# Optimization experiments

Measured on AMD Instinct MI355X. Metric: run time of the kernel, lower is better.

## Reference

```python
import jax, jax.numpy as jnp
import numpy as np

N, E, H, S = 50000, 400000, 128, 3  # nodes, edges, hidden_dim, mp steps
NODE_IN, EDGE_IN, OUT = 4, 3, 2


def _mlp(x, W1, b1, W2, b2, W3, b3):
    # MLP(in, [H, H], out): Linear->ReLU->Linear->ReLU->Linear
    h = jax.nn.relu(x @ W1 + b1)
    h = jax.nn.relu(h @ W2 + b2)
    return h @ W3 + b3


def setup_inputs() -> dict:
    key = jax.random.key(0)
    ks = iter(jax.random.split(key, 64))

    def p(shape):
        fan_in = shape[-2]
        return (jax.random.normal(next(ks), shape, jnp.float32) / np.float32(np.sqrt(fan_in)))

    inp = {}
    inp["x"] = jax.random.normal(next(ks), (N, NODE_IN), jnp.float32)
    inp["edge_attr"] = jax.random.normal(next(ks), (E, EDGE_IN), jnp.float32)
    inp["edge_index"] = jax.random.randint(next(ks), (2, E), 0, N, jnp.int32)
    # node encoder MLP(NODE_IN,[H,H],H)
    inp["ne_W1"], inp["ne_b1"] = p((NODE_IN, H)), jnp.zeros((H,), jnp.float32)
    inp["ne_W2"], inp["ne_b2"] = p((H, H)), jnp.zeros((H,), jnp.float32)
    inp["ne_W3"], inp["ne_b3"] = p((H, H)), jnp.zeros((H,), jnp.float32)
    # edge encoder MLP(EDGE_IN,[H,H],H)
    inp["ee_W1"], inp["ee_b1"] = p((EDGE_IN, H)), jnp.zeros((H,), jnp.float32)
    inp["ee_W2"], inp["ee_b2"] = p((H, H)), jnp.zeros((H,), jnp.float32)
    inp["ee_W3"], inp["ee_b3"] = p((H, H)), jnp.zeros((H,), jnp.float32)
    # processor: per-step edge MLP(3H,[H,H],H) and node MLP(2H,[H,H],H), stacked over S
    inp["pe_W1"], inp["pe_b1"] = p((S, 3 * H, H)), jnp.zeros((S, H), jnp.float32)
    inp["pe_W2"], inp["pe_b2"] = p((S, H, H)), jnp.zeros((S, H), jnp.float32)
    inp["pe_W3"], inp["pe_b3"] = p((S, H, H)), jnp.zeros((S, H), jnp.float32)
    inp["pn_W1"], inp["pn_b1"] = p((S, 2 * H, H)), jnp.zeros((S, H), jnp.float32)
    inp["pn_W2"], inp["pn_b2"] = p((S, H, H)), jnp.zeros((S, H), jnp.float32)
    inp["pn_W3"], inp["pn_b3"] = p((S, H, H)), jnp.zeros((S, H), jnp.float32)
    # node decoder MLP(H,[H,H],OUT)
    inp["nd_W1"], inp["nd_b1"] = p((H, H)), jnp.zeros((H,), jnp.float32)
    inp["nd_W2"], inp["nd_b2"] = p((H, H)), jnp.zeros((H,), jnp.float32)
    inp["nd_W3"], inp["nd_b3"] = p((H, OUT)), jnp.zeros((OUT,), jnp.float32)
    return inp


def reference(x, edge_attr, edge_index,
              ne_W1, ne_b1, ne_W2, ne_b2, ne_W3, ne_b3,
              ee_W1, ee_b1, ee_W2, ee_b2, ee_W3, ee_b3,
              pe_W1, pe_b1, pe_W2, pe_b2, pe_W3, pe_b3,
              pn_W1, pn_b1, pn_W2, pn_b2, pn_W3, pn_b3,
              nd_W1, nd_b1, nd_W2, nd_b2, nd_W3, nd_b3):
    src, dst = edge_index[0], edge_index[1]
    # encode
    h = _mlp(x, ne_W1, ne_b1, ne_W2, ne_b2, ne_W3, ne_b3)          # [N, H]
    e = _mlp(edge_attr, ee_W1, ee_b1, ee_W2, ee_b2, ee_W3, ee_b3)  # [E, H]
    # processor: gather -> edge MLP (residual) -> scatter-sum -> node MLP (residual)
    for t in range(S):
        m_in = jnp.concatenate([h[src], h[dst], e], axis=-1)        # [E, 3H]
        e = e + _mlp(m_in, pe_W1[t], pe_b1[t], pe_W2[t], pe_b2[t], pe_W3[t], pe_b3[t])
        agg = jax.ops.segment_sum(e, dst, num_segments=N)           # [N, H]
        n_in = jnp.concatenate([h, agg], axis=-1)                   # [N, 2H]
        h = h + _mlp(n_in, pn_W1[t], pn_b1[t], pn_W2[t], pn_b2[t], pn_W3[t], pn_b3[t])
    # decode
    return _mlp(h, nd_W1, nd_b1, nd_W2, nd_b2, nd_W3, nd_b3)        # [N, OUT]
```

## Files before the change

kernel.cpp:

```cpp
#include <hip/hip_runtime.h>
#include <hip/hip_bf16.h>
#include <cstddef>

#define NND 50000
#define NNDP 50048
#define NED 400000
#define HD 128
#define NSTEP 3
#define NSB 196
#define NWP 32

using u16 = unsigned short;
typedef __attribute__((ext_vector_type(8))) short bf16x8;
typedef __attribute__((ext_vector_type(4))) float f32x4;

__device__ __forceinline__ u16 f2b(float f) {
    __hip_bfloat16 b = __float2bfloat16(f);
    union { __hip_bfloat16 b; u16 u; } v; v.b = b;
    return v.u;
}
__device__ __forceinline__ float b2f(u16 u) {
    union { unsigned u; float f; } v; v.u = ((unsigned)u) << 16;
    return v.f;
}

template <int RT>
__device__ __forceinline__ void zero_accs(f32x4 (&acc)[RT][4]) {
    #pragma unroll
    for (int g = 0; g < RT; g++)
        #pragma unroll
        for (int i = 0; i < 4; i++) acc[g][i] = (f32x4)(0.0f);
}

__device__ __forceinline__ void mfma4T(bf16x8 act, const bf16x8 (&wf)[4], f32x4 (&accr)[4]) {
    accr[0] = __builtin_amdgcn_mfma_f32_16x16x32_bf16(wf[0], act, accr[0], 0, 0, 0);
    accr[1] = __builtin_amdgcn_mfma_f32_16x16x32_bf16(wf[1], act, accr[1], 0, 0, 0);
    accr[2] = __builtin_amdgcn_mfma_f32_16x16x32_bf16(wf[2], act, accr[2], 0, 0, 0);
    accr[3] = __builtin_amdgcn_mfma_f32_16x16x32_bf16(wf[3], act, accr[3], 0, 0, 0);
}

__device__ __forceinline__ void load_w16(const u16* __restrict__ Wf, int wc, int lane,
                                         bf16x8 (&wB)[16]) {
    const u16* bp = Wf + (size_t)(wc * 16) * 512 + lane * 8;
    #pragma unroll
    for (int i = 0; i < 16; i++) wB[i] = *(const bf16x8*)(bp + i * 512);
}

template <int RT>
__device__ __forceinline__ void gemm_reg_T(const u16* t, int rbase, const bf16x8 (&wB)[16],
                                           int lane, f32x4 (&acc)[RT][4]) {
    const int cl = lane & 15, q8 = (lane >> 4) * 8;
    #pragma unroll
    for (int k0 = 0; k0 < 4; k0++) {
        const bf16x8 wf[4] = {wB[k0], wB[4 + k0], wB[8 + k0], wB[12 + k0]};
        #pragma unroll
        for (int rt = 0; rt < RT; rt++) {
            bf16x8 a = *(const bf16x8*)(t + (rbase + rt * 16 + cl) * 136 + k0 * 32 + q8);
            mfma4T(a, wf, acc[rt]);
        }
    }
}

template <int KC, int RT>
__device__ __forceinline__ void gemm_lds_T(const u16* t, int rbase,
                                           const u16* __restrict__ Wf,
                                           int wc, int lane, f32x4 (&acc)[RT][4]) {
    const int cl = lane & 15, q8 = (lane >> 4) * 8;
    const u16* bp = Wf + (size_t)(wc * 4 * KC) * 512 + lane * 8;
    #pragma unroll
    for (int k0 = 0; k0 < KC; k0++) {
        bf16x8 wf[4];
        #pragma unroll
        for (int ct = 0; ct < 4; ct++) wf[ct] = *(const bf16x8*)(bp + (ct * KC + k0) * 512);
        #pragma unroll
        for (int rt = 0; rt < RT; rt++) {
            bf16x8 a = *(const bf16x8*)(t + (rbase + rt * 16 + cl) * 136 + k0 * 32 + q8);
            mfma4T(a, wf, acc[rt]);
        }
    }
}

template <int RT, bool RELU>
__device__ __forceinline__ void store_T(u16* T, int rbase, int wc, int lane,
        const f32x4 (&acc)[RT][4], const float* __restrict__ bias) {
    const int cl = lane & 15, q = lane >> 4;
    float4 bv[4];
    #pragma unroll
    for (int ct = 0; ct < 4; ct++)
        bv[ct] = *(const float4*)(bias + wc * 64 + ct * 16 + q * 4);
    #pragma unroll
    for (int rt = 0; rt < RT; rt++) {
        const int row = rbase + rt * 16 + cl;
        #pragma unroll
        for (int ct = 0; ct < 4; ct++) {
            float v0 = acc[rt][ct][0] + bv[ct].x;
            float v1 = acc[rt][ct][1] + bv[ct].y;
            float v2 = acc[rt][ct][2] + bv[ct].z;
            float v3 = acc[rt][ct][3] + bv[ct].w;
            if (RELU) {
                v0 = fmaxf(v0, 0.f); v1 = fmaxf(v1, 0.f);
                v2 = fmaxf(v2, 0.f); v3 = fmaxf(v3, 0.f);
            }
            uint2 pk;
            pk.x = (unsigned)f2b(v0) | ((unsigned)f2b(v1) << 16);
            pk.y = (unsigned)f2b(v2) | ((unsigned)f2b(v3) << 16);
            *(uint2*)(T + row * 136 + wc * 64 + ct * 16 + q * 4) = pk;
        }
    }
}

template <int RT>
__device__ __forceinline__ void store_T_perm(u16* T, int rbase, int wc, int lane,
        const f32x4 (&acc)[RT][4]) {
    const int cl = lane & 15, q = lane >> 4;
    #pragma unroll
    for (int rt = 0; rt < RT; rt++) {
        const int row = rbase + rt * 16 + cl;
        #pragma unroll
        for (int ct = 0; ct < 4; ct++) {
            uint2 pk;
            pk.x = (unsigned)f2b(acc[rt][ct][0]) | ((unsigned)f2b(acc[rt][ct][1]) << 16);
            pk.y = (unsigned)f2b(acc[rt][ct][2]) | ((unsigned)f2b(acc[rt][ct][3]) << 16);
            *(uint2*)(T + row * 136 + wc * 64 + q * 16 + ct * 4) = pk;
        }
    }
}

template <int RT>
__device__ __forceinline__ void epi_plain(const u16* T, u16* __restrict__ base, int row0,
        int rbase, int nrows, int wc, int lane) {
    #pragma unroll
    for (int p = 0; p < RT * 2; p++) {
        const int lrow = rbase + p * 8 + (lane >> 3);
        const int col = wc * 64 + (lane & 7) * 8;
        const int grow = row0 + lrow;
        if (grow < nrows) {
            bf16x8 tv = *(const bf16x8*)(T + lrow * 136 + col);
            *(bf16x8*)(base + (size_t)grow * HD + col) = tv;
        }
    }
}

__global__ void count_kernel(const int* __restrict__ eidx, int* __restrict__ counts) {
    int i = blockIdx.x * 256 + threadIdx.x;
    if (i < NED) atomicAdd(&counts[eidx[NED + i]], 1);
}

__global__ __launch_bounds__(256) void bsum_kernel(const int* __restrict__ counts,
                                                   int* __restrict__ bsum) {
    __shared__ int sm[256];
    const int i = threadIdx.x, b = blockIdx.x;
    const int idx = b * 256 + i;
    sm[i] = (idx < NNDP) ? counts[idx] : 0;
    __syncthreads();
    for (int ofs = 128; ofs > 0; ofs >>= 1) {
        if (i < ofs) sm[i] += sm[i + ofs];
        __syncthreads();
    }
    if (i == 0) bsum[b] = sm[0];
}

__global__ __launch_bounds__(256) void bscan_kernel(const int* __restrict__ bsum,
                                                    int* __restrict__ bbase,
                                                    int* __restrict__ offsets) {
    __shared__ int sm[256];
    const int i = threadIdx.x;
    int v = (i < NSB) ? bsum[i] : 0;
    sm[i] = v;
    __syncthreads();
    for (int ofs = 1; ofs < 256; ofs <<= 1) {
        int t = (i >= ofs) ? sm[i - ofs] : 0;
        __syncthreads();
        sm[i] += t;
        __syncthreads();
    }
    if (i < NSB) bbase[i] = sm[i] - v;
    if (i == NSB - 1) offsets[NNDP] = sm[i];
}

__global__ __launch_bounds__(256) void blocal_kernel(const int* __restrict__ counts,
                                                     const int* __restrict__ bbase,
                                                     int* __restrict__ offsets,
                                                     int* __restrict__ cursors) {
    __shared__ int sm[256];
    const int i = threadIdx.x, b = blockIdx.x;
    const int idx = b * 256 + i;
    int v = (idx < NNDP) ? counts[idx] : 0;
    sm[i] = v;
    __syncthreads();
    for (int ofs = 1; ofs < 256; ofs <<= 1) {
        int t = (i >= ofs) ? sm[i - ofs] : 0;
        __syncthreads();
        sm[i] += t;
        __syncthreads();
    }
    if (idx < NNDP) {
        int excl = sm[i] - v + bbase[b];
        offsets[idx] = excl;
        cursors[idx] = excl;
    }
}

__global__ void fill_kernel(const int* __restrict__ eidx, int* __restrict__ cursors,
                            int4* __restrict__ epk) {
    int i = blockIdx.x * 256 + threadIdx.x;
    if (i >= NED) return;
    int d = eidx[NED + i];
    int pos = atomicAdd(&cursors[d], 1);
    int4 v; v.x = eidx[i]; v.y = d; v.z = i; v.w = 0;
    epk[pos] = v;
}

struct WPall {
    const float* s[NWP];
    u16* d[NWP];
    int K[NWP];
    int Kp[NWP];
};

__global__ void wprep_all(WPall a) {
    const int wi = blockIdx.y;
    const int Kp = a.Kp[wi];
    int idx = blockIdx.x * 256 + threadIdx.x;
    if (idx >= 128 * Kp) return;
    const int K = a.K[wi];
    const float* __restrict__ src = a.s[wi];
    int j = idx & 7, lane = (idx >> 3) & 63, rest = idx >> 9;
    int KC = Kp >> 5;
    int k0 = rest % KC, n0 = rest / KC;
    int n = n0 * 16 + (lane & 15);
    int k = k0 * 32 + (lane >> 4) * 8 + j;
    float v = (k < K) ? src[(size_t)k * 128 + n] : 0.0f;
    a.d[wi][idx] = f2b(v);
}

__global__ __launch_bounds__(256, 2) void pnode_mfma(
    const u16* __restrict__ h,
    const u16* __restrict__ WsF, const u16* __restrict__ WdF,
    u16* __restrict__ Ps, u16* __restrict__ Pd) {
    __shared__ u16 t1[64 * 136];
    const int tid = threadIdx.x;
    const int lane = tid & 63, w = tid >> 6, wr = w >> 1, wc = w & 1;
    const int cl = lane & 15, q8 = (lane >> 4) * 8;
    const int row0 = blockIdx.x * 64;
    const int rbase = wr * 32;

    bf16x8 aA[2][4];
    #pragma unroll
    for (int rt = 0; rt < 2; rt++) {
        const u16* hp = h + (size_t)(row0 + rbase + rt * 16 + cl) * HD + q8;
        #pragma unroll
        for (int k0 = 0; k0 < 4; k0++) aA[rt][k0] = *(const bf16x8*)(hp + k0 * 32);
    }
    bf16x8 wB[16];
    f32x4 acc[2][4];

    load_w16(WsF, wc, lane, wB);
    zero_accs<2>(acc);
    #pragma unroll
    for (int k0 = 0; k0 < 4; k0++) {
        const bf16x8 wf[4] = {wB[k0], wB[4 + k0], wB[8 + k0], wB[12 + k0]};
        #pragma unroll
        for (int rt = 0; rt < 2; rt++) mfma4T(aA[rt][k0], wf, acc[rt]);
    }
    store_T_perm<2>(t1, rbase, wc, lane, acc);
    epi_plain<2>(t1, Ps, row0, rbase, NNDP, wc, lane);

    load_w16(WdF, wc, lane, wB);
    zero_accs<2>(acc);
    #pragma unroll
    for (int k0 = 0; k0 < 4; k0++) {
        const bf16x8 wf[4] = {wB[k0], wB[4 + k0], wB[8 + k0], wB[12 + k0]};
        #pragma unroll
        for (int rt = 0; rt < 2; rt++) mfma4T(aA[rt][k0], wf, acc[rt]);
    }
    store_T_perm<2>(t1, rbase, wc, lane, acc);
    epi_plain<2>(t1, Pd, row0, rbase, NNDP, wc, lane);
}

__global__ __launch_bounds__(256, 4) void enc_mfma(
    const float* __restrict__ in, int Kin, int nrows, const int4* __restrict__ epk,
    const u16* __restrict__ W1f, const float* __restrict__ b1,
    const u16* __restrict__ W2f, const float* __restrict__ b2,
    const u16* __restrict__ W3f, const float* __restrict__ b3,
    u16* __restrict__ out) {
    __shared__ u16 t1[64 * 136];
    __shared__ u16 t2[64 * 136];
    const int tid = threadIdx.x;
    const int lane = tid & 63, w = tid >> 6, wr = w >> 1, wc = w & 1;
    const int cl = lane & 15, q8 = (lane >> 4) * 8;
    const int row0 = blockIdx.x * 64;
    const int rbase = wr * 32;

    f32x4 acc[2][4];
    zero_accs<2>(acc);
    bf16x8 a[2];
    #pragma unroll
    for (int rt = 0; rt < 2; rt++) {
        a[rt] = (bf16x8){0, 0, 0, 0, 0, 0, 0, 0};
        int grow = row0 + rbase + rt * 16 + cl;
        if (q8 == 0 && grow < nrows) {
            int irow = epk ? epk[grow].z : grow;
            const float* xr = in + (size_t)irow * Kin;
            if (Kin == 4) {
                float4 v = *(const float4*)xr;
                a[rt][0] = (short)f2b(v.x); a[rt][1] = (short)f2b(v.y);
                a[rt][2] = (short)f2b(v.z); a[rt][3] = (short)f2b(v.w);
            } else {
                a[rt][0] = (short)f2b(xr[0]); a[rt][1] = (short)f2b(xr[1]);
                a[rt][2] = (short)f2b(xr[2]);
            }
        }
    }
    {
        const u16* b1p = W1f + (size_t)(wc * 4) * 512 + lane * 8;
        bf16x8 wf[4];
        #pragma unroll
        for (int ct = 0; ct < 4; ct++) wf[ct] = *(const bf16x8*)(b1p + ct * 512);
        #pragma unroll
        for (int rt = 0; rt < 2; rt++) mfma4T(a[rt], wf, acc[rt]);
    }
    store_T<2, true>(t1, rbase, wc, lane, acc, b1);
    __syncthreads();
    zero_accs<2>(acc);
    gemm_lds_T<4, 2>(t1, rbase, W2f, wc, lane, acc);
    store_T<2, true>(t2, rbase, wc, lane, acc, b2);
    __syncthreads();
    zero_accs<2>(acc);
    gemm_lds_T<4, 2>(t2, rbase, W3f, wc, lane, acc);
    store_T<2, false>(t1, rbase, wc, lane, acc, b3);
    epi_plain<2>(t1, out, row0, rbase, nrows, wc, lane);
}

__global__ __launch_bounds__(256, 2) void edge_mfma(
    u16* __restrict__ e, const int4* __restrict__ epk,
    const u16* __restrict__ Ps, const u16* __restrict__ Pd,
    const u16* __restrict__ W1eF, const float* __restrict__ b1,
    const u16* __restrict__ W2f, const float* __restrict__ b2,
    const u16* __restrict__ W3f, const float* __restrict__ b3) {
    __shared__ u16 t1[128 * 136];
    __shared__ u16 t2[128 * 136];
    const int tid = threadIdx.x;
    const int lane = tid & 63, w = tid >> 6, wr = w >> 1, wc = w & 1;
    const int cl = lane & 15, q = lane >> 4, q8 = q * 8;
    const int row0 = blockIdx.x * 128;
    const int rbase = wr * 64;

    bf16x8 wB[16];
    load_w16(W2f, wc, lane, wB);

    int srcv[4], dstv[4];
    const u16* epv[4];
    #pragma unroll
    for (int rt = 0; rt < 4; rt++) {
        int myrow = row0 + rbase + rt * 16 + cl;
        int4 pk = epk[myrow];
        srcv[rt] = pk.x; dstv[rt] = pk.y;
        epv[rt] = e + (size_t)myrow * HD + q8;
    }

    const int pofs = wc * 64 + q * 16;
    f32x4 acc[4][4];
    #pragma unroll
    for (int rt = 0; rt < 4; rt++) {
        const u16* ps = Ps + (size_t)srcv[rt] * HD + pofs;
        const u16* pd = Pd + (size_t)dstv[rt] * HD + pofs;
        bf16x8 a0 = *(const bf16x8*)ps;
        bf16x8 a1 = *(const bf16x8*)(ps + 8);
        bf16x8 b0 = *(const bf16x8*)pd;
        bf16x8 b1v = *(const bf16x8*)(pd + 8);
        #pragma unroll
        for (int ct = 0; ct < 2; ct++)
            #pragma unroll
            for (int i = 0; i < 4; i++)
                acc[rt][ct][i] = b2f((u16)a0[ct * 4 + i]) + b2f((u16)b0[ct * 4 + i]);
        #pragma unroll
        for (int ct = 2; ct < 4; ct++)
            #pragma unroll
            for (int i = 0; i < 4; i++)
                acc[rt][ct][i] = b2f((u16)a1[(ct - 2) * 4 + i]) + b2f((u16)b1v[(ct - 2) * 4 + i]);
    }
    const u16* b1p = W1eF + (size_t)(wc * 16) * 512 + lane * 8;
    #pragma unroll
    for (int k0 = 0; k0 < 4; k0++) {
        bf16x8 wf[4];
        #pragma unroll
        for (int ct = 0; ct < 4; ct++) wf[ct] = *(const bf16x8*)(b1p + (ct * 4 + k0) * 512);
        #pragma unroll
        for (int rt = 0; rt < 4; rt++) {
            bf16x8 a = *(const bf16x8*)(epv[rt] + k0 * 32);
            mfma4T(a, wf, acc[rt]);
        }
    }
    store_T<4, true>(t1, rbase, wc, lane, acc, b1);
    __syncthreads();
    zero_accs<4>(acc);
    gemm_reg_T<4>(t1, rbase, wB, lane, acc);
    load_w16(W3f, wc, lane, wB);
    store_T<4, true>(t2, rbase, wc, lane, acc, b2);
    __syncthreads();
    bf16x8 eold[8];
    #pragma unroll
    for (int p = 0; p < 8; p++) {
        const int lrow = rbase + p * 8 + (lane >> 3);
        const int col = wc * 64 + (lane & 7) * 8;
        eold[p] = *(const bf16x8*)(e + (size_t)(row0 + lrow) * HD + col);
    }
    zero_accs<4>(acc);
    gemm_reg_T<4>(t2, rbase, wB, lane, acc);
    store_T<4, false>(t1, rbase, wc, lane, acc, b3);
    #pragma unroll
    for (int p = 0; p < 8; p++) {
        const int lrow = rbase + p * 8 + (lane >> 3);
        const int col = wc * 64 + (lane & 7) * 8;
        bf16x8 tv = *(const bf16x8*)(t1 + lrow * 136 + col);
        bf16x8 res;
        #pragma unroll
        for (int k = 0; k < 8; k++)
            res[k] = (short)f2b(b2f((u16)tv[k]) + b2f((u16)eold[p][k]));
        *(bf16x8*)(e + (size_t)(row0 + lrow) * HD + col) = res;
    }
}

__global__ __launch_bounds__(256, 3) void node_mfma(
    u16* __restrict__ h, const u16* __restrict__ e, const int* __restrict__ offsets,
    const u16* __restrict__ W1f, const float* __restrict__ b1,
    const u16* __restrict__ W2f, const float* __restrict__ b2,
    const u16* __restrict__ W3f, const float* __restrict__ b3,
    const u16* __restrict__ W1sNx, const u16* __restrict__ W1dNx,
    u16* __restrict__ Ps, u16* __restrict__ Pd) {
    __shared__ u16 tb[64 * 136];
    __shared__ u16 aggT[64 * 136];
    const int tid = threadIdx.x;
    const int lane = tid & 63, w = tid >> 6, wr = w >> 1, wc = w & 1;
    const int cl = lane & 15, q8 = (lane >> 4) * 8;
    const int row0 = blockIdx.x * 64;
    const int rbase = wr * 32;

    {
        const int r = tid >> 2, sgi = tid & 3;
        const int node = row0 + r;
        const int beg = offsets[node], end = offsets[node + 1];
        float s[32];
        #pragma unroll
        for (int k = 0; k < 32; k++) s[k] = 0.0f;
        const u16* ebase = e + sgi * 32;
        int j = beg;
        for (; j + 2 <= end; j += 2) {
            const bf16x8* e0 = (const bf16x8*)(ebase + (size_t)j * HD);
            const bf16x8* e1 = (const bf16x8*)(ebase + (size_t)(j + 1) * HD);
            bf16x8 v0 = e0[0], v1 = e0[1], v2 = e0[2], v3 = e0[3];
            bf16x8 u0 = e1[0], u1 = e1[1], u2 = e1[2], u3 = e1[3];
            #pragma unroll
            for (int k = 0; k < 8; k++) {
                s[k]      += b2f((u16)v0[k]) + b2f((u16)u0[k]);
                s[8 + k]  += b2f((u16)v1[k]) + b2f((u16)u1[k]);
                s[16 + k] += b2f((u16)v2[k]) + b2f((u16)u2[k]);
                s[24 + k] += b2f((u16)v3[k]) + b2f((u16)u3[k]);
            }
        }
        if (j < end) {
            const bf16x8* e0 = (const bf16x8*)(ebase + (size_t)j * HD);
            bf16x8 v0 = e0[0], v1 = e0[1], v2 = e0[2], v3 = e0[3];
            #pragma unroll
            for (int k = 0; k < 8; k++) {
                s[k]      += b2f((u16)v0[k]);
                s[8 + k]  += b2f((u16)v1[k]);
                s[16 + k] += b2f((u16)v2[k]);
                s[24 + k] += b2f((u16)v3[k]);
            }
        }
        #pragma unroll
        for (int q = 0; q < 4; q++) {
            bf16x8 o;
            #pragma unroll
            for (int k = 0; k < 8; k++) o[k] = (short)f2b(s[q * 8 + k]);
            *(bf16x8*)(aggT + r * 136 + sgi * 32 + q * 8) = o;
        }
    }
    __syncthreads();

    f32x4 acc[2][4];
    zero_accs<2>(acc);
    const u16* b1p = W1f + (size_t)(wc * 32) * 512 + lane * 8;
    const u16* hp[2];
    #pragma unroll
    for (int rt = 0; rt < 2; rt++)
        hp[rt] = h + (size_t)(row0 + rbase + rt * 16 + cl) * HD + q8;
    #pragma unroll
    for (int k0 = 0; k0 < 4; k0++) {
        bf16x8 wf[4];
        #pragma unroll
        for (int ct = 0; ct < 4; ct++) wf[ct] = *(const bf16x8*)(b1p + (ct * 8 + k0) * 512);
        #pragma unroll
        for (int rt = 0; rt < 2; rt++) {
            bf16x8 a = *(const bf16x8*)(hp[rt] + k0 * 32);
            mfma4T(a, wf, acc[rt]);
        }
    }
    #pragma unroll
    for (int k0 = 0; k0 < 4; k0++) {
        bf16x8 wf[4];
        #pragma unroll
        for (int ct = 0; ct < 4; ct++) wf[ct] = *(const bf16x8*)(b1p + (ct * 8 + 4 + k0) * 512);
        #pragma unroll
        for (int rt = 0; rt < 2; rt++) {
            bf16x8 a = *(const bf16x8*)(aggT + (rbase + rt * 16 + cl) * 136 + k0 * 32 + q8);
            mfma4T(a, wf, acc[rt]);
        }
    }
    store_T<2, true>(tb, rbase, wc, lane, acc, b1);
    __syncthreads();
    zero_accs<2>(acc);
    gemm_lds_T<4, 2>(tb, rbase, W2f, wc, lane, acc);
    store_T<2, true>(aggT, rbase, wc, lane, acc, b2);
    __syncthreads();
    bf16x8 hold[4];
    #pragma unroll
    for (int p = 0; p < 4; p++) {
        const int lrow = rbase + p * 8 + (lane >> 3);
        const int col = wc * 64 + (lane & 7) * 8;
        hold[p] = *(const bf16x8*)(h + (size_t)(row0 + lrow) * HD + col);
    }
    zero_accs<2>(acc);
    gemm_lds_T<4, 2>(aggT, rbase, W3f, wc, lane, acc);
    store_T<2, false>(tb, rbase, wc, lane, acc, b3);
    #pragma unroll
    for (int p = 0; p < 4; p++) {
        const int lrow = rbase + p * 8 + (lane >> 3);
        const int col = wc * 64 + (lane & 7) * 8;
        bf16x8 tv = *(const bf16x8*)(tb + lrow * 136 + col);
        bf16x8 res;
        #pragma unroll
        for (int k = 0; k < 8; k++)
            res[k] = (short)f2b(b2f((u16)tv[k]) + b2f((u16)hold[p][k]));
        *(bf16x8*)(h + (size_t)(row0 + lrow) * HD + col) = res;
        *(bf16x8*)(tb + lrow * 136 + col) = res;
    }
    if (W1sNx) {
        __syncthreads();
        bf16x8 wB[16];
        load_w16(W1sNx, wc, lane, wB);
        f32x4 pac[2][4];
        zero_accs<2>(pac);
        gemm_reg_T<2>(tb, rbase, wB, lane, pac);
        store_T_perm<2>(aggT, rbase, wc, lane, pac);
        epi_plain<2>(aggT, Ps, row0, rbase, NNDP, wc, lane);
        load_w16(W1dNx, wc, lane, wB);
        zero_accs<2>(pac);
        gemm_reg_T<2>(tb, rbase, wB, lane, pac);
        store_T_perm<2>(aggT, rbase, wc, lane, pac);
        epi_plain<2>(aggT, Pd, row0, rbase, NNDP, wc, lane);
    }
}

__global__ __launch_bounds__(256, 4) void dec_mfma(
    const u16* __restrict__ h,
    const u16* __restrict__ W1f, const float* __restrict__ b1,
    const u16* __restrict__ W2f, const float* __restrict__ b2,
    const float* __restrict__ W3, const float* __restrict__ b3,
    float* __restrict__ out) {
    __shared__ u16 t1[32 * 136];
    __shared__ u16 t2[32 * 136];
    const int tid = threadIdx.x;
    const int lane = tid & 63, w = tid >> 6, wr = w >> 1, wc = w & 1;
    const int cl = lane & 15, q8 = (lane >> 4) * 8;
    const int row0 = blockIdx.x * 32;
    const int rbase = wr * 16;
    const u16* hp = h + (size_t)(row0 + rbase + cl) * HD + q8;

    f32x4 acc[1][4];
    zero_accs<1>(acc);
    const u16* b1p = W1f + (size_t)(wc * 16) * 512 + lane * 8;
    #pragma unroll
    for (int k0 = 0; k0 < 4; k0++) {
        bf16x8 wf[4];
        #pragma unroll
        for (int ct = 0; ct < 4; ct++) wf[ct] = *(const bf16x8*)(b1p + (ct * 4 + k0) * 512);
        bf16x8 a = *(const bf16x8*)(hp + k0 * 32);
        mfma4T(a, wf, acc[0]);
    }
    store_T<1, true>(t1, rbase, wc, lane, acc, b1);
    __syncthreads();
    zero_accs<1>(acc);
    gemm_lds_T<4, 1>(t1, rbase, W2f, wc, lane, acc);
    store_T<1, true>(t2, rbase, wc, lane, acc, b2);
    __syncthreads();
    if (tid < 64) {
        const int rr = tid >> 1, o = tid & 1;
        const int grow = row0 + rr;
        if (grow < NND) {
            float a = b3[o];
            for (int k = 0; k < HD; k++) a += b2f(t2[rr * 136 + k]) * W3[k * 2 + o];
            out[(size_t)grow * 2 + o] = a;
        }
    }
}

extern "C" void kernel_launch(void* const* d_in, const int* in_sizes, int n_in,
                              void* d_out, int out_size, void* d_ws, size_t ws_size,
                              hipStream_t stream) {
    (void)in_sizes; (void)n_in; (void)out_size; (void)ws_size;
    const float* x    = (const float*)d_in[0];
    const float* eatt = (const float*)d_in[1];
    const int*   eidx = (const int*)d_in[2];
    const float *neW1 = (const float*)d_in[3],  *neb1 = (const float*)d_in[4];
    const float *neW2 = (const float*)d_in[5],  *neb2 = (const float*)d_in[6];
    const float *neW3 = (const float*)d_in[7],  *neb3 = (const float*)d_in[8];
    const float *eeW1 = (const float*)d_in[9],  *eeb1 = (const float*)d_in[10];
    const float *eeW2 = (const float*)d_in[11], *eeb2 = (const float*)d_in[12];
    const float *eeW3 = (const float*)d_in[13], *eeb3 = (const float*)d_in[14];
    const float *peW1 = (const float*)d_in[15], *peb1 = (const float*)d_in[16];
    const float *peW2 = (const float*)d_in[17], *peb2 = (const float*)d_in[18];
    const float *peW3 = (const float*)d_in[19], *peb3 = (const float*)d_in[20];
    const float *pnW1 = (const float*)d_in[21], *pnb1 = (const float*)d_in[22];
    const float *pnW2 = (const float*)d_in[23], *pnb2 = (const float*)d_in[24];
    const float *pnW3 = (const float*)d_in[25], *pnb3 = (const float*)d_in[26];
    const float *ndW1 = (const float*)d_in[27], *ndb1 = (const float*)d_in[28];
    const float *ndW2 = (const float*)d_in[29], *ndb2 = (const float*)d_in[30];
    const float *ndW3 = (const float*)d_in[31], *ndb3 = (const float*)d_in[32];

    char* ws = (char*)d_ws;
    u16*   h       = (u16*)ws;
    u16*   e       = (u16*)(ws + 12812288);
    int*   bsum    = (int*)(ws + 115212288);
    int*   bbase   = (int*)(ws + 115213312);
    int*   counts  = (int*)(ws + 115245056);
    int*   cursors = (int*)(ws + 115445248);
    int*   offsets = (int*)(ws + 115645440);
    int4*  epk     = (int4*)(ws + 115845760);
    u16*   Ps      = (u16*)(ws + 122245760);
    u16*   Pd      = (u16*)(ws + 135058048);
    u16*   wts     = (u16*)(ws + 147870336);

    u16* p = wts;
    u16 *neW1t = p; p += 128 * 32;
    u16 *neW2t = p; p += 128 * 128;
    u16 *neW3t = p; p += 128 * 128;
    u16 *eeW1t = p; p += 128 * 32;
    u16 *eeW2t = p; p += 128 * 128;
    u16 *eeW3t = p; p += 128 * 128;
    u16 *peW1sF[NSTEP], *peW1dF[NSTEP], *peW1eF[NSTEP], *peW2t[NSTEP], *peW3t[NSTEP];
    u16 *pnW1t[NSTEP], *pnW2t[NSTEP], *pnW3t[NSTEP];
    for (int t = 0; t < NSTEP; t++) {
        peW1sF[t] = p; p += 128 * 128;
        peW1dF[t] = p; p += 128 * 128;
        peW1eF[t] = p; p += 128 * 128;
        peW2t[t]  = p; p += 128 * 128;
        peW3t[t]  = p; p += 128 * 128;
    }
    for (int t = 0; t < NSTEP; t++) {
        pnW1t[t] = p; p += 128 * 256;
        pnW2t[t] = p; p += 128 * 128;
        pnW3t[t] = p; p += 128 * 128;
    }
    u16 *ndW1t = p; p += 128 * 128;
    u16 *ndW2t = p; p += 128 * 128;

    hipMemsetAsync(counts, 0, NNDP * sizeof(int), stream);
    count_kernel<<<(NED + 255) / 256, 256, 0, stream>>>(eidx, counts);
    bsum_kernel<<<NSB, 256, 0, stream>>>(counts, bsum);
    bscan_kernel<<<1, 256, 0, stream>>>(bsum, bbase, offsets);
    blocal_kernel<<<NSB, 256, 0, stream>>>(counts, bbase, offsets, cursors);
    fill_kernel<<<(NED + 255) / 256, 256, 0, stream>>>(eidx, cursors, epk);

    WPall wa;
    int wn = 0;
    auto ADD = [&](const float* s, u16* d, int K, int Kp) {
        wa.s[wn] = s; wa.d[wn] = d; wa.K[wn] = K; wa.Kp[wn] = Kp; wn++;
    };
    ADD(neW1, neW1t, 4, 32);
    ADD(neW2, neW2t, 128, 128);
    ADD(neW3, neW3t, 128, 128);
    ADD(eeW1, eeW1t, 3, 32);
    ADD(eeW2, eeW2t, 128, 128);
    ADD(eeW3, eeW3t, 128, 128);
    for (int t = 0; t < NSTEP; t++) {
        const float* base = peW1 + (size_t)t * 384 * 128;
        ADD(base,             peW1sF[t], 128, 128);
        ADD(base + 128 * 128, peW1dF[t], 128, 128);
        ADD(base + 256 * 128, peW1eF[t], 128, 128);
        ADD(peW2 + (size_t)t * 128 * 128, peW2t[t], 128, 128);
        ADD(peW3 + (size_t)t * 128 * 128, peW3t[t], 128, 128);
        ADD(pnW1 + (size_t)t * 256 * 128, pnW1t[t], 256, 256);
        ADD(pnW2 + (size_t)t * 128 * 128, pnW2t[t], 128, 128);
        ADD(pnW3 + (size_t)t * 128 * 128, pnW3t[t], 128, 128);
    }
    ADD(ndW1, ndW1t, 128, 128);
    ADD(ndW2, ndW2t, 128, 128);
    wprep_all<<<dim3(128, NWP), 256, 0, stream>>>(wa);

    enc_mfma<<<NNDP / 64, 256, 0, stream>>>(x, 4, NND, nullptr,
                                            neW1t, neb1, neW2t, neb2, neW3t, neb3, h);
    enc_mfma<<<NED / 64, 256, 0, stream>>>(eatt, 3, NED, epk,
                                           eeW1t, eeb1, eeW2t, eeb2, eeW3t, eeb3, e);
    pnode_mfma<<<NNDP / 64, 256, 0, stream>>>(h, peW1sF[0], peW1dF[0], Ps, Pd);

    for (int t = 0; t < NSTEP; t++) {
        edge_mfma<<<NED / 128, 256, 0, stream>>>(
            e, epk, Ps, Pd,
            peW1eF[t], peb1 + (size_t)t * HD,
            peW2t[t],  peb2 + (size_t)t * HD,
            peW3t[t],  peb3 + (size_t)t * HD);
        const bool last = (t + 1 == NSTEP);
        node_mfma<<<NNDP / 64, 256, 0, stream>>>(
            h, e, offsets,
            pnW1t[t], pnb1 + (size_t)t * HD,
            pnW2t[t], pnb2 + (size_t)t * HD,
            pnW3t[t], pnb3 + (size_t)t * HD,
            last ? nullptr : peW1sF[t + 1],
            last ? nullptr : peW1dF[t + 1],
            Ps, Pd);
    }
    dec_mfma<<<NNDP / 32, 256, 0, stream>>>(h, ndW1t, ndb1, ndW2t, ndb2, ndW3, ndb3, (float*)d_out);
}
```

Baseline: 531.3 us.

## Fuse scatter-sum into edge kernel via atomics into fp32 aggregation buffer

The edge kernel now writes its updated edge rows into shared memory and accumulates runs of equal destination (edges appear sorted by dst) into a global fp32 agg buffer with atomicAdd. The node kernel then reads the precomputed aggregation instead of re-reading all edge rows through CSR offsets. This is meant to remove the second pass over the 400k x 128 edge tensor, at the cost of a memset of agg each step, float atomics and extra barriers in the edge kernel.

After: 816.2 us. +53.6%, slower.

```diff
diff --git a/kernel.cpp b/kernel.cpp
--- a/kernel.cpp
+++ b/kernel.cpp
@@ -335,16 +335,20 @@
 __global__ __launch_bounds__(256, 2) void edge_mfma(
     u16* __restrict__ e, const int4* __restrict__ epk,
     const u16* __restrict__ Ps, const u16* __restrict__ Pd,
+    float* __restrict__ agg,
     const u16* __restrict__ W1eF, const float* __restrict__ b1,
     const u16* __restrict__ W2f, const float* __restrict__ b2,
     const u16* __restrict__ W3f, const float* __restrict__ b3) {
     __shared__ u16 t1[128 * 136];
     __shared__ u16 t2[128 * 136];
+    __shared__ int dsts_l[128];
     const int tid = threadIdx.x;
     const int lane = tid & 63, w = tid >> 6, wr = w >> 1, wc = w & 1;
     const int cl = lane & 15, q = lane >> 4, q8 = q * 8;
     const int row0 = blockIdx.x * 128;
     const int rbase = wr * 64;
+
+    if (tid < 128) dsts_l[tid] = epk[row0 + tid].y;
 
     bf16x8 wB[16];
     load_w16(W2f, wc, lane, wB);
@@ -409,6 +413,7 @@
     zero_accs<4>(acc);
     gemm_reg_T<4>(t2, rbase, wB, lane, acc);
     store_T<4, false>(t1, rbase, wc, lane, acc, b3);
+    __syncthreads();
     #pragma unroll
     for (int p = 0; p < 8; p++) {
         const int lrow = rbase + p * 8 + (lane >> 3);
@@ -419,11 +424,36 @@
         for (int k = 0; k < 8; k++)
             res[k] = (short)f2b(b2f((u16)tv[k]) + b2f((u16)eold[p][k]));
         *(bf16x8*)(e + (size_t)(row0 + lrow) * HD + col) = res;
+        *(bf16x8*)(t2 + lrow * 136 + col) = res;
+    }
+    __syncthreads();
+    {
+        const int cs = (tid & 31) * 4;
+        const int r0a = (tid >> 5) * 16;
+        float s0 = 0.f, s1 = 0.f, s2 = 0.f, s3 = 0.f;
+        int cur = dsts_l[r0a];
+        for (int r = 0; r < 16; r++) {
+            const int rr = r0a + r;
+            const int d = dsts_l[rr];
+            if (d != cur) {
+                float* ap = agg + (size_t)cur * HD + cs;
+                atomicAdd(ap + 0, s0); atomicAdd(ap + 1, s1);
+                atomicAdd(ap + 2, s2); atomicAdd(ap + 3, s3);
+                s0 = s1 = s2 = s3 = 0.f;
+                cur = d;
+            }
+            uint2 pk = *(const uint2*)(t2 + rr * 136 + cs);
+            s0 += b2f((u16)(pk.x & 0xFFFF)); s1 += b2f((u16)(pk.x >> 16));
+            s2 += b2f((u16)(pk.y & 0xFFFF)); s3 += b2f((u16)(pk.y >> 16));
+        }
+        float* ap = agg + (size_t)cur * HD + cs;
+        atomicAdd(ap + 0, s0); atomicAdd(ap + 1, s1);
+        atomicAdd(ap + 2, s2); atomicAdd(ap + 3, s3);
     }
 }
 
 __global__ __launch_bounds__(256, 3) void node_mfma(
-    u16* __restrict__ h, const u16* __restrict__ e, const int* __restrict__ offsets,
+    u16* __restrict__ h, const float* __restrict__ agg,
     const u16* __restrict__ W1f, const float* __restrict__ b1,
     const u16* __restrict__ W2f, const float* __restrict__ b2,
     const u16* __restrict__ W3f, const float* __restrict__ b3,
@@ -439,43 +469,17 @@
 
     {
         const int r = tid >> 2, sgi = tid & 3;
-        const int node = row0 + r;
-        const int beg = offsets[node], end = offsets[node + 1];
-        float s[32];
-        #pragma unroll
-        for (int k = 0; k < 32; k++) s[k] = 0.0f;
-        const u16* ebase = e + sgi * 32;
-        int j = beg;
-        for (; j + 2 <= end; j += 2) {
-            const bf16x8* e0 = (const bf16x8*)(ebase + (size_t)j * HD);
-            const bf16x8* e1 = (const bf16x8*)(ebase + (size_t)(j + 1) * HD);
-            bf16x8 v0 = e0[0], v1 = e0[1], v2 = e0[2], v3 = e0[3];
-            bf16x8 u0 = e1[0], u1 = e1[1], u2 = e1[2], u3 = e1[3];
-            #pragma unroll
-            for (int k = 0; k < 8; k++) {
-                s[k]      += b2f((u16)v0[k]) + b2f((u16)u0[k]);
-                s[8 + k]  += b2f((u16)v1[k]) + b2f((u16)u1[k]);
-                s[16 + k] += b2f((u16)v2[k]) + b2f((u16)u2[k]);
-                s[24 + k] += b2f((u16)v3[k]) + b2f((u16)u3[k]);
-            }
-        }
-        if (j < end) {
-            const bf16x8* e0 = (const bf16x8*)(ebase + (size_t)j * HD);
-            bf16x8 v0 = e0[0], v1 = e0[1], v2 = e0[2], v3 = e0[3];
-            #pragma unroll
-            for (int k = 0; k < 8; k++) {
-                s[k]      += b2f((u16)v0[k]);
-                s[8 + k]  += b2f((u16)v1[k]);
-                s[16 + k] += b2f((u16)v2[k]);
-                s[24 + k] += b2f((u16)v3[k]);
-            }
-        }
-        #pragma unroll
-        for (int q = 0; q < 4; q++) {
+        const float* ap = agg + (size_t)(row0 + r) * HD + sgi * 32;
+        #pragma unroll
+        for (int qq = 0; qq < 4; qq++) {
+            float4 f0 = *(const float4*)(ap + qq * 8);
+            float4 f1 = *(const float4*)(ap + qq * 8 + 4);
             bf16x8 o;
-            #pragma unroll
-            for (int k = 0; k < 8; k++) o[k] = (short)f2b(s[q * 8 + k]);
-            *(bf16x8*)(aggT + r * 136 + sgi * 32 + q * 8) = o;
+            o[0] = (short)f2b(f0.x); o[1] = (short)f2b(f0.y);
+            o[2] = (short)f2b(f0.z); o[3] = (short)f2b(f0.w);
+            o[4] = (short)f2b(f1.x); o[5] = (short)f2b(f1.y);
+            o[6] = (short)f2b(f1.z); o[7] = (short)f2b(f1.w);
+            *(bf16x8*)(aggT + r * 136 + sgi * 32 + qq * 8) = o;
         }
     }
     __syncthreads();
@@ -631,7 +635,8 @@
     int4*  epk     = (int4*)(ws + 115845760);
     u16*   Ps      = (u16*)(ws + 122245760);
     u16*   Pd      = (u16*)(ws + 135058048);
-    u16*   wts     = (u16*)(ws + 147870336);
+    float* agg     = (float*)(ws + 147870336);
+    u16*   wts     = (u16*)(ws + 173494912);
 
     u16* p = wts;
     u16 *neW1t = p; p += 128 * 32;
@@ -697,14 +702,15 @@
     pnode_mfma<<<NNDP / 64, 256, 0, stream>>>(h, peW1sF[0], peW1dF[0], Ps, Pd);
 
     for (int t = 0; t < NSTEP; t++) {
+        hipMemsetAsync(agg, 0, (size_t)NNDP * HD * sizeof(float), stream);
         edge_mfma<<<NED / 128, 256, 0, stream>>>(
-            e, epk, Ps, Pd,
+            e, epk, Ps, Pd, agg,
             peW1eF[t], peb1 + (size_t)t * HD,
             peW2t[t],  peb2 + (size_t)t * HD,
             peW3t[t],  peb3 + (size_t)t * HD);
         const bool last = (t + 1 == NSTEP);
         node_mfma<<<NNDP / 64, 256, 0, stream>>>(
-            h, e, offsets,
+            h, agg,
             pnW1t[t], pnb1 + (size_t)t * HD,
             pnW2t[t], pnb2 + (size_t)t * HD,
             pnW3t[t], pnb3 + (size_t)t * HD,
```
